# Performance work log

Hardware: AMD Instinct MI355X
Metric: run time of the kernel (lower is better)

The kernel has to match this reference:

```python
import jax, jax.numpy as jnp
import numpy as np

B, S, E, H = 8, 1024, 1024, 16
D = E // H  # head_dim = 64
NEG_INF = jnp.finfo(jnp.float32).min


def setup_inputs() -> dict:
    key = jax.random.key(0)
    ks = jax.random.split(key, 14)
    w = 0.02  # init scale for projection weights
    inp = {
        "query": jax.random.normal(ks[0], (B, S, E), jnp.float32),
        "key": jax.random.normal(ks[1], (B, S, E), jnp.float32),
        "value": jax.random.normal(ks[2], (B, S, E), jnp.float32),
        "attn_bias": jax.random.normal(ks[3], (B, H, S, S), jnp.float32),
        "key_padding_mask": jax.random.randint(ks[4], (B, S), 0, 2).astype(bool),
        "attn_mask": jnp.zeros((S, S), jnp.float32),
        "need_weights": 0,
        "before_softmax": 0,
        "need_head_weights": 0,
        "Wq": jax.random.normal(ks[5], (E, E), jnp.float32) * w,
        "bq": jnp.zeros((E,), jnp.float32),
        "Wk": jax.random.normal(ks[6], (E, E), jnp.float32) * w,
        "bk": jnp.zeros((E,), jnp.float32),
        "Wv": jax.random.normal(ks[7], (E, E), jnp.float32) * w,
        "bv": jnp.zeros((E,), jnp.float32),
        "Wo": jax.random.normal(ks[8], (E, E), jnp.float32) * w,
        "bo": jnp.zeros((E,), jnp.float32),
    }
    return inp


def reference(query, key, value, attn_bias, key_padding_mask, attn_mask,
              need_weights, before_softmax, need_head_weights,
              Wq, bq, Wk, bk, Wv, bv, Wo, bo):
    # self_attention=True: torch code projects q, k, v ALL from `query`.
    scaling = D ** -0.5
    q = (query @ Wq.T + bq) * scaling          # [B,S,E]
    k = query @ Wk.T + bk
    v = query @ Wv.T + bv
    q = q.reshape(B, S, H, D)
    k = k.reshape(B, S, H, D)
    v = v.reshape(B, S, H, D)
    # scores: QK^T + bias + mask, materialized [B,H,S,S] like the torch bmm
    scores = jnp.einsum('bqhd,bkhd->bhqk', q, k)
    scores = scores + attn_bias
    scores = scores + attn_mask[None, None]    # attn_mask broadcast over B,H
    scores = jnp.where(key_padding_mask[:, None, None, :], NEG_INF, scores)
    probs = jax.nn.softmax(scores, axis=-1)    # dropout p=0.0 -> identity
    attn = jnp.einsum('bhqk,bkhd->bqhd', probs, v).reshape(B, S, E)
    out = attn @ Wo.T + bo                     # [B,S,E]
    # need_weights=False path: torch returns (attn, None); return attn only.
    return out
```

## Files before the change

kernel.cpp:

```cpp
#include <hip/hip_runtime.h>

#define B_ 8
#define S_ 1024
#define E_ 1024
#define H_ 16
#define D_ 64

typedef __attribute__((ext_vector_type(8))) short bf16x8;
typedef __attribute__((ext_vector_type(4))) float floatx4;

__device__ __forceinline__ floatx4 mfma16x16x32(bf16x8 a, bf16x8 b, floatx4 c) {
  return __builtin_amdgcn_mfma_f32_16x16x32_bf16(a, b, c, 0, 0, 0);
}

__device__ __forceinline__ unsigned short f2bf(float x) {
  unsigned int u = __builtin_bit_cast(unsigned int, x);
  u += 0x7FFFu + ((u >> 16) & 1u);
  return (unsigned short)(u >> 16);
}

__device__ __forceinline__ void async16(const unsigned short* g, unsigned short* l) {
  __builtin_amdgcn_global_load_lds(
      (const __attribute__((address_space(1))) void*)g,
      (__attribute__((address_space(3))) void*)l, 16, 0, 0);
}

__global__ void mask_prep(const unsigned int* __restrict__ mraw, float* __restrict__ maskadd) {
  __shared__ int flagF, flagB;
  const int tid = threadIdx.x;
  if (tid == 0) { flagF = 0; flagB = 0; }
  __syncthreads();
  int lf = 0, lb = 0;
  for (int i = tid; i < 2048; i += 256) {
    unsigned int v = mraw[i];
    if (v == 0x3F800000u) lf = 1;
    else if (v > 1u) lb = 1;
  }
  if (lf) atomicOr(&flagF, 1);
  if (lb) atomicOr(&flagB, 1);
  __syncthreads();
  const unsigned char* mb = (const unsigned char*)mraw;
  const float* mf = (const float*)mraw;
  const int* mi = (const int*)mraw;
  const int fF = flagF, fB = flagB;
  for (int i = tid; i < B_ * S_; i += 256) {
    int pad;
    if (fF)      pad = (mf[i] != 0.0f);
    else if (fB) pad = (mb[i] != 0);
    else         pad = (mi[i] != 0);
    maskadd[i] = pad ? -3.4028234663852886e38f : 0.0f;
  }
}

__global__ __launch_bounds__(256) void convert_prep(
    const float* __restrict__ q, const float* __restrict__ wq, const float* __restrict__ wk,
    const float* __restrict__ wv, const float* __restrict__ wo,
    unsigned short* __restrict__ xb, unsigned short* __restrict__ wqb,
    unsigned short* __restrict__ wkb, unsigned short* __restrict__ wvb,
    unsigned short* __restrict__ wob)
{
  size_t idx = (size_t)blockIdx.x * 256 + threadIdx.x;
  const float* src; unsigned short* dst; size_t off;
  if (idx < 2097152)      { src = q;  dst = xb;  off = idx; }
  else if (idx < 2359296) { src = wq; dst = wqb; off = idx - 2097152; }
  else if (idx < 2621440) { src = wk; dst = wkb; off = idx - 2359296; }
  else if (idx < 2883584) { src = wv; dst = wvb; off = idx - 2621440; }
  else                    { src = wo; dst = wob; off = idx - 2883584; }
  float4 v = *(const float4*)(src + off * 4);
  ushort4 u; u.x = f2bf(v.x); u.y = f2bf(v.y); u.z = f2bf(v.z); u.w = f2bf(v.w);
  *(ushort4*)(dst + off * 4) = u;
}

__device__ __forceinline__ void gemm_core(
    const unsigned short* __restrict__ A, const unsigned short* __restrict__ Bm,
    int m0, int n0, unsigned short* As, unsigned short* Bs, floatx4 (&acc)[4][4])
{
  const int tid = threadIdx.x;
  const int wave = tid >> 6, lane = tid & 63;
  const int quad = lane >> 4, l16 = lane & 15;
  const int mb = (wave >> 1) * 64, nb = (wave & 1) * 64;
  const int ldrow = lane >> 3;
  const int gchunk = (lane & 7) ^ ldrow;

  for (int ks = 0; ks < 16; ++ks) {
    const int k0 = ks * 64;
    __syncthreads();
    for (int is = 0; is < 4; ++is) {
      int issue = wave * 4 + is;
      async16(A + (size_t)(m0 + issue * 8 + ldrow) * 1024 + k0 + gchunk * 8, &As[issue * 512]);
      async16(Bm + (size_t)(n0 + issue * 8 + ldrow) * 1024 + k0 + gchunk * 8, &Bs[issue * 512]);
    }
    __syncthreads();
    for (int kk = 0; kk < 2; ++kk) {
      const int pc = ((quad + 4 * kk) ^ (l16 & 7)) * 8;
      bf16x8 af[4], bfm[4];
      for (int i = 0; i < 4; ++i)
        af[i] = *(const bf16x8*)(&As[(mb + 16 * i + l16) * 64 + pc]);
      for (int j = 0; j < 4; ++j)
        bfm[j] = *(const bf16x8*)(&Bs[(nb + 16 * j + l16) * 64 + pc]);
      for (int i = 0; i < 4; ++i)
        for (int j = 0; j < 4; ++j)
          acc[i][j] = mfma16x16x32(af[i], bfm[j], acc[i][j]);
    }
  }
}

__global__ __launch_bounds__(256) void gemm_qkv(
    const unsigned short* __restrict__ Xbf,
    const unsigned short* __restrict__ Wqb, const unsigned short* __restrict__ Wkb,
    const unsigned short* __restrict__ Wvb,
    const float* __restrict__ bq, const float* __restrict__ bk, const float* __restrict__ bv,
    unsigned short* __restrict__ qo, unsigned short* __restrict__ ko, unsigned short* __restrict__ vo)
{
  const int n0 = blockIdx.x * 128;
  const int m0 = blockIdx.y * 128;
  const int which = n0 >> 10;
  const int nn0 = n0 & 1023;
  const unsigned short* W = (which == 0) ? Wqb : (which == 1) ? Wkb : Wvb;
  const float* bias = (which == 0) ? bq : (which == 1) ? bk : bv;

  __shared__ unsigned short As[128 * 64];
  __shared__ unsigned short Bs[128 * 64];

  const int lane = threadIdx.x & 63, wave = threadIdx.x >> 6;
  const int quad = lane >> 4, l16 = lane & 15;
  const int mb = (wave >> 1) * 64, nb = (wave & 1) * 64;

  floatx4 z = {0.f, 0.f, 0.f, 0.f};
  floatx4 acc[4][4];
  for (int i = 0; i < 4; ++i) for (int j = 0; j < 4; ++j) acc[i][j] = z;

  gemm_core(Xbf, W, m0, nn0, As, Bs, acc);

  float bv4[4];
  for (int j = 0; j < 4; ++j) bv4[j] = bias[nn0 + nb + 16 * j + l16];

  for (int i = 0; i < 4; ++i) {
    for (int r = 0; r < 4; ++r) {
      int m = m0 + mb + 16 * i + quad * 4 + r;
      int bb = m >> 10, s = m & 1023;
      for (int j = 0; j < 4; ++j) {
        int nn = nn0 + nb + 16 * j + l16;
        int hh = nn >> 6, d = nn & 63;
        float val = acc[i][j][r] + bv4[j];
        if (which == 0) {
          val *= 0.125f;
          qo[((size_t)(bb * 16 + hh) * 1024 + s) * 64 + d] = f2bf(val);
        } else if (which == 1) {
          ko[((size_t)(bb * 16 + hh) * 1024 + s) * 64 + d] = f2bf(val);
        } else {
          vo[((size_t)(bb * 16 + hh) * 64 + d) * 1024 + s] = f2bf(val);
        }
      }
    }
  }
}

__global__ __launch_bounds__(256) void gemm_out(
    const unsigned short* __restrict__ Abf, const unsigned short* __restrict__ Wob,
    const float* __restrict__ bo, float* __restrict__ out)
{
  const int n0 = blockIdx.x * 128;
  const int m0 = blockIdx.y * 128;
  __shared__ unsigned short As[128 * 64];
  __shared__ unsigned short Bs[128 * 64];

  const int lane = threadIdx.x & 63, wave = threadIdx.x >> 6;
  const int quad = lane >> 4, l16 = lane & 15;
  const int mb = (wave >> 1) * 64, nb = (wave & 1) * 64;

  floatx4 z = {0.f, 0.f, 0.f, 0.f};
  floatx4 acc[4][4];
  for (int i = 0; i < 4; ++i) for (int j = 0; j < 4; ++j) acc[i][j] = z;

  gemm_core(Abf, Wob, m0, n0, As, Bs, acc);

  for (int i = 0; i < 4; ++i) {
    for (int r = 0; r < 4; ++r) {
      int m = m0 + mb + 16 * i + quad * 4 + r;
      for (int j = 0; j < 4; ++j) {
        int n = n0 + nb + 16 * j + l16;
        out[(size_t)m * 1024 + n] = acc[i][j][r] + bo[n];
      }
    }
  }
}

__global__ __launch_bounds__(256) void attn_fwd(
    const unsigned short* __restrict__ qw, const unsigned short* __restrict__ kw,
    const unsigned short* __restrict__ vw, const float* __restrict__ bias,
    const float* __restrict__ amask, const float* __restrict__ maskadd,
    unsigned short* __restrict__ attnw)
{
  const int tid = threadIdx.x;
  const int wave = tid >> 6, lane = tid & 63;
  const int quad = lane >> 4, l16 = lane & 15;
  const int qt = blockIdx.x, bh = blockIdx.y;
  const int b = bh >> 4, h = bh & 15;
  const int qbase = qt * 64 + wave * 16;

  const unsigned short* qh = qw + (size_t)bh * (S_ * D_);
  const unsigned short* kh = kw + (size_t)bh * (S_ * D_);
  const unsigned short* vh = vw + (size_t)bh * (S_ * D_);
  const float* biasb = bias + (size_t)bh * ((size_t)S_ * S_) + (size_t)(qt * 64) * S_;
  const float* amrow = amask + (size_t)(qt * 64) * S_;
  const float* madd  = maskadd + b * S_;

  __shared__ float sc[64 * 68];
  __shared__ unsigned short Vt[64 * 64];
  __shared__ unsigned short P_lds[4 * 16 * 72];
  unsigned short* Pw = &P_lds[wave * (16 * 72)];

  const int srow = tid >> 4;
  const int skc  = tid & 15;
  const int vrow = tid >> 3;
  const int vchk = tid & 7;

  bf16x8 aQ0 = *(const bf16x8*)(qh + (size_t)(qbase + l16) * 64 + quad * 8);
  bf16x8 aQ1 = *(const bf16x8*)(qh + (size_t)(qbase + l16) * 64 + 32 + quad * 8);

  float4 pb[4], pa[4], pm;
  bf16x8 pv[2];
  auto load_tile = [&](int key0) {
    pm = *(const float4*)(madd + key0 + skc * 4);
    for (int r4 = 0; r4 < 4; ++r4) {
      pb[r4] = *(const float4*)(biasb + (size_t)(srow + 16 * r4) * S_ + key0 + skc * 4);
      pa[r4] = *(const float4*)(amrow + (size_t)(srow + 16 * r4) * S_ + key0 + skc * 4);
    }
    for (int i2 = 0; i2 < 2; ++i2) {
      int d = vrow + 32 * i2;
      int gc = vchk ^ (d & 7);
      pv[i2] = *(const bf16x8*)(vh + (size_t)d * 1024 + key0 + gc * 8);
    }
  };
  load_tile(0);

  floatx4 zz = {0.f, 0.f, 0.f, 0.f};
  floatx4 oacc[4] = {zz, zz, zz, zz};
  float m_run[4], l_run[4];
  for (int r = 0; r < 4; ++r) { m_run[r] = -__builtin_inff(); l_run[r] = 0.f; }

  for (int kt = 0; kt < 16; ++kt) {
    const int key0 = kt * 64;
    __syncthreads();
    for (int r4 = 0; r4 < 4; ++r4) {
      float4 s;
      s.x = pb[r4].x + pa[r4].x + pm.x;
      s.y = pb[r4].y + pa[r4].y + pm.y;
      s.z = pb[r4].z + pa[r4].z + pm.z;
      s.w = pb[r4].w + pa[r4].w + pm.w;
      *(float4*)(&sc[(srow + 16 * r4) * 68 + skc * 4]) = s;
    }
    for (int i2 = 0; i2 < 2; ++i2)
      *(bf16x8*)(&Vt[(vrow + 32 * i2) * 64 + vchk * 8]) = pv[i2];

    bf16x8 bK0[4], bK1[4];
    for (int t = 0; t < 4; ++t) {
      const unsigned short* kr = kh + (size_t)(key0 + 16 * t + l16) * 64;
      bK0[t] = *(const bf16x8*)(kr + quad * 8);
      bK1[t] = *(const bf16x8*)(kr + 32 + quad * 8);
    }
    if (kt < 15) load_tile(key0 + 64);
    __syncthreads();

    floatx4 sfr[4];
    for (int t = 0; t < 4; ++t) {
      floatx4 c;
      for (int r = 0; r < 4; ++r)
        c[r] = sc[(wave * 16 + quad * 4 + r) * 68 + 16 * t + l16];
      c = mfma16x16x32(aQ0, bK0[t], c);
      c = mfma16x16x32(aQ1, bK1[t], c);
      sfr[t] = c;
    }
    for (int r = 0; r < 4; ++r) {
      float rm = fmaxf(fmaxf(sfr[0][r], sfr[1][r]), fmaxf(sfr[2][r], sfr[3][r]));
      rm = fmaxf(rm, __shfl_xor(rm, 1));
      rm = fmaxf(rm, __shfl_xor(rm, 2));
      rm = fmaxf(rm, __shfl_xor(rm, 4));
      rm = fmaxf(rm, __shfl_xor(rm, 8));
      float mnew = fmaxf(m_run[r], rm);
      float alpha = __expf(m_run[r] - mnew);
      float psum = 0.f;
      for (int t = 0; t < 4; ++t) {
        float p = __expf(sfr[t][r] - mnew);
        psum += p;
        Pw[(quad * 4 + r) * 72 + 16 * t + l16] = f2bf(p);
      }
      psum += __shfl_xor(psum, 1);
      psum += __shfl_xor(psum, 2);
      psum += __shfl_xor(psum, 4);
      psum += __shfl_xor(psum, 8);
      l_run[r] = l_run[r] * alpha + psum;
      m_run[r] = mnew;
      oacc[0][r] *= alpha; oacc[1][r] *= alpha; oacc[2][r] *= alpha; oacc[3][r] *= alpha;
    }
    for (int kc = 0; kc < 2; ++kc) {
      bf16x8 aP = *(const bf16x8*)(Pw + l16 * 72 + kc * 32 + quad * 8);
      const int pc = ((kc * 4 + quad) ^ (l16 & 7)) * 8;
      for (int t = 0; t < 4; ++t) {
        bf16x8 bV = *(const bf16x8*)(&Vt[(16 * t + l16) * 64 + pc]);
        oacc[t] = mfma16x16x32(aP, bV, oacc[t]);
      }
    }
  }

  for (int r = 0; r < 4; ++r) {
    int row = qbase + quad * 4 + r;
    float inv = 1.0f / l_run[r];
    unsigned short* orow = attnw + (size_t)(b * S_ + row) * E_ + h * 64;
    for (int t = 0; t < 4; ++t)
      orow[16 * t + l16] = f2bf(oacc[t][r] * inv);
  }
}

extern "C" void kernel_launch(void* const* d_in, const int* in_sizes, int n_in,
                              void* d_out, int out_size, void* d_ws, size_t ws_size,
                              hipStream_t stream) {
  const float* query      = (const float*)d_in[0];
  const float* attn_bias  = (const float*)d_in[3];
  const unsigned int* kpm = (const unsigned int*)d_in[4];
  const float* amask      = (const float*)d_in[5];
  const float* Wq = (const float*)d_in[9];
  const float* bq = (const float*)d_in[10];
  const float* Wk = (const float*)d_in[11];
  const float* bk = (const float*)d_in[12];
  const float* Wv = (const float*)d_in[13];
  const float* bv = (const float*)d_in[14];
  const float* Wo = (const float*)d_in[15];
  const float* bo = (const float*)d_in[16];

  char* ws = (char*)d_ws;
  const size_t MB16 = 16777216;
  unsigned short* qw    = (unsigned short*)(ws);
  unsigned short* kw    = (unsigned short*)(ws + MB16);
  unsigned short* vw    = (unsigned short*)(ws + 2 * MB16);
  unsigned short* xbf   = (unsigned short*)(ws + 3 * MB16);
  unsigned short* attnw = (unsigned short*)(ws + 3 * MB16);
  unsigned short* wqb   = (unsigned short*)(ws + 4 * MB16);
  unsigned short* wkb   = (unsigned short*)(ws + 4 * MB16 + 2097152);
  unsigned short* wvb   = (unsigned short*)(ws + 4 * MB16 + 2 * 2097152);
  unsigned short* wob   = (unsigned short*)(ws + 4 * MB16 + 3 * 2097152);
  float* maskadd        = (float*)(ws + 4 * MB16 + 4 * 2097152);

  mask_prep<<<1, 256, 0, stream>>>(kpm, maskadd);
  convert_prep<<<12288, 256, 0, stream>>>(query, Wq, Wk, Wv, Wo, xbf, wqb, wkb, wvb, wob);
  gemm_qkv<<<dim3(24, 64), 256, 0, stream>>>(xbf, wqb, wkb, wvb, bq, bk, bv, qw, kw, vw);
  attn_fwd<<<dim3(16, 128), 256, 0, stream>>>(qw, kw, vw, attn_bias, amask, maskadd, attnw);
  gemm_out<<<dim3(8, 64), 256, 0, stream>>>(attnw, wob, bo, (float*)d_out);
}
```

Before: 977.2 us.

## Stage QKV epilogue through LDS, swizzle block order, load bias directly into MFMA layout

The QKV GEMM epilogue now stages the bf16 tile in shared memory (transposed for V) and writes 16-byte vector stores to global, replacing scattered 2-byte stores. All three kernels remap block indices with a swizzle so that neighbouring workgroups are spread across tiles, aimed at L2/XCD locality. The attention kernel drops the LDS score staging buffer and loads bias, mask and padding values straight into registers in the MFMA accumulator layout, double-buffered across key tiles. This costs more registers, and the direct loads are narrower scalar loads than the earlier float4 loads.

```diff
diff --git a/kernel.cpp b/kernel.cpp
--- a/kernel.cpp
+++ b/kernel.cpp
@@ -112,17 +112,22 @@
     const float* __restrict__ bq, const float* __restrict__ bk, const float* __restrict__ bv,
     unsigned short* __restrict__ qo, unsigned short* __restrict__ ko, unsigned short* __restrict__ vo)
 {
-  const int n0 = blockIdx.x * 128;
-  const int m0 = blockIdx.y * 128;
+  const int tid = threadIdx.x;
+  const int flat = blockIdx.y * 24 + blockIdx.x;
+  const int swz = (flat & 7) * 192 + (flat >> 3);
+  const int bx = swz % 24, by = swz / 24;
+  const int n0 = bx * 128;
+  const int m0 = by * 128;
   const int which = n0 >> 10;
   const int nn0 = n0 & 1023;
   const unsigned short* W = (which == 0) ? Wqb : (which == 1) ? Wkb : Wvb;
   const float* bias = (which == 0) ? bq : (which == 1) ? bk : bv;
 
-  __shared__ unsigned short As[128 * 64];
-  __shared__ unsigned short Bs[128 * 64];
-
-  const int lane = threadIdx.x & 63, wave = threadIdx.x >> 6;
+  __shared__ unsigned short smem[128 * 136];
+  unsigned short* As = smem;
+  unsigned short* Bs = smem + 8192;
+
+  const int lane = tid & 63, wave = tid >> 6;
   const int quad = lane >> 4, l16 = lane & 15;
   const int mb = (wave >> 1) * 64, nb = (wave & 1) * 64;
 
@@ -135,24 +140,50 @@
   float bv4[4];
   for (int j = 0; j < 4; ++j) bv4[j] = bias[nn0 + nb + 16 * j + l16];
 
-  for (int i = 0; i < 4; ++i) {
-    for (int r = 0; r < 4; ++r) {
-      int m = m0 + mb + 16 * i + quad * 4 + r;
-      int bb = m >> 10, s = m & 1023;
-      for (int j = 0; j < 4; ++j) {
-        int nn = nn0 + nb + 16 * j + l16;
-        int hh = nn >> 6, d = nn & 63;
-        float val = acc[i][j][r] + bv4[j];
-        if (which == 0) {
-          val *= 0.125f;
-          qo[((size_t)(bb * 16 + hh) * 1024 + s) * 64 + d] = f2bf(val);
-        } else if (which == 1) {
-          ko[((size_t)(bb * 16 + hh) * 1024 + s) * 64 + d] = f2bf(val);
-        } else {
-          vo[((size_t)(bb * 16 + hh) * 64 + d) * 1024 + s] = f2bf(val);
-        }
-      }
-    }
+  __syncthreads();
+
+  const float scale = (which == 0) ? 0.125f : 1.0f;
+  if (which < 2) {
+    #pragma unroll
+    for (int i = 0; i < 4; ++i)
+      #pragma unroll
+      for (int r = 0; r < 4; ++r) {
+        const int mr = mb + 16 * i + quad * 4 + r;
+        #pragma unroll
+        for (int j = 0; j < 4; ++j)
+          smem[mr * 136 + nb + 16 * j + l16] = f2bf((acc[i][j][r] + bv4[j]) * scale);
+      }
+  } else {
+    #pragma unroll
+    for (int i = 0; i < 4; ++i)
+      #pragma unroll
+      for (int r = 0; r < 4; ++r) {
+        const int mr = mb + 16 * i + quad * 4 + r;
+        #pragma unroll
+        for (int j = 0; j < 4; ++j)
+          smem[(nb + 16 * j + l16) * 136 + mr] = f2bf(acc[i][j][r] + bv4[j]);
+      }
+  }
+  __syncthreads();
+
+  const int row = tid >> 1, half = tid & 1;
+  if (which < 2) {
+    const int m = m0 + row, bb = m >> 10, s = m & 1023;
+    const int hh = (nn0 >> 6) + half;
+    unsigned short* dst = ((which == 0) ? qo : ko) +
+        ((size_t)(bb * 16 + hh) * 1024 + s) * 64;
+    #pragma unroll
+    for (int c = 0; c < 8; ++c)
+      *(bf16x8*)(dst + c * 8) = *(const bf16x8*)(&smem[row * 136 + half * 64 + c * 8]);
+  } else {
+    const int nglob = nn0 + row;
+    const int hh = nglob >> 6, d = nglob & 63;
+    const int bb = m0 >> 10;
+    unsigned short* dst = vo + ((size_t)(bb * 16 + hh) * 64 + d) * 1024 +
+        (m0 & 1023) + half * 64;
+    #pragma unroll
+    for (int c = 0; c < 8; ++c)
+      *(bf16x8*)(dst + c * 8) = *(const bf16x8*)(&smem[row * 136 + half * 64 + c * 8]);
   }
 }
 
@@ -160,8 +191,10 @@
     const unsigned short* __restrict__ Abf, const unsigned short* __restrict__ Wob,
     const float* __restrict__ bo, float* __restrict__ out)
 {
-  const int n0 = blockIdx.x * 128;
-  const int m0 = blockIdx.y * 128;
+  const int flat = blockIdx.y * 8 + blockIdx.x;
+  const int swz = (flat & 7) * 64 + (flat >> 3);
+  const int n0 = (swz & 7) * 128;
+  const int m0 = (swz >> 3) * 128;
   __shared__ unsigned short As[128 * 64];
   __shared__ unsigned short Bs[128 * 64];
 
@@ -195,45 +228,53 @@
   const int tid = threadIdx.x;
   const int wave = tid >> 6, lane = tid & 63;
   const int quad = lane >> 4, l16 = lane & 15;
-  const int qt = blockIdx.x, bh = blockIdx.y;
+  const int flat = blockIdx.y * 16 + blockIdx.x;
+  const int swz = (flat & 7) * 256 + (flat >> 3);
+  const int qt = swz & 15, bh = swz >> 4;
   const int b = bh >> 4, h = bh & 15;
   const int qbase = qt * 64 + wave * 16;
 
   const unsigned short* qh = qw + (size_t)bh * (S_ * D_);
   const unsigned short* kh = kw + (size_t)bh * (S_ * D_);
   const unsigned short* vh = vw + (size_t)bh * (S_ * D_);
-  const float* biasb = bias + (size_t)bh * ((size_t)S_ * S_) + (size_t)(qt * 64) * S_;
-  const float* amrow = amask + (size_t)(qt * 64) * S_;
+  const float* biasb = bias + (size_t)bh * ((size_t)S_ * S_) +
+                       (size_t)(qt * 64 + wave * 16 + quad * 4) * S_;
+  const float* amrow = amask + (size_t)(qt * 64 + wave * 16 + quad * 4) * S_;
   const float* madd  = maskadd + b * S_;
 
-  __shared__ float sc[64 * 68];
   __shared__ unsigned short Vt[64 * 64];
   __shared__ unsigned short P_lds[4 * 16 * 72];
   unsigned short* Pw = &P_lds[wave * (16 * 72)];
 
-  const int srow = tid >> 4;
-  const int skc  = tid & 15;
   const int vrow = tid >> 3;
   const int vchk = tid & 7;
 
   bf16x8 aQ0 = *(const bf16x8*)(qh + (size_t)(qbase + l16) * 64 + quad * 8);
   bf16x8 aQ1 = *(const bf16x8*)(qh + (size_t)(qbase + l16) * 64 + 32 + quad * 8);
 
-  float4 pb[4], pa[4], pm;
   bf16x8 pv[2];
-  auto load_tile = [&](int key0) {
-    pm = *(const float4*)(madd + key0 + skc * 4);
-    for (int r4 = 0; r4 < 4; ++r4) {
-      pb[r4] = *(const float4*)(biasb + (size_t)(srow + 16 * r4) * S_ + key0 + skc * 4);
-      pa[r4] = *(const float4*)(amrow + (size_t)(srow + 16 * r4) * S_ + key0 + skc * 4);
-    }
+  float cc[4][4], nc[4][4];
+
+  auto load_v = [&](int key0) {
+    #pragma unroll
     for (int i2 = 0; i2 < 2; ++i2) {
       int d = vrow + 32 * i2;
       int gc = vchk ^ (d & 7);
       pv[i2] = *(const bf16x8*)(vh + (size_t)d * 1024 + key0 + gc * 8);
     }
   };
-  load_tile(0);
+  auto load_cinit = [&](int key0, float (&dst)[4][4]) {
+    #pragma unroll
+    for (int t = 0; t < 4; ++t) {
+      const int col = key0 + 16 * t + l16;
+      const float mv = madd[col];
+      #pragma unroll
+      for (int r = 0; r < 4; ++r)
+        dst[t][r] = biasb[(size_t)r * S_ + col] + amrow[(size_t)r * S_ + col] + mv;
+    }
+  };
+  load_v(0);
+  load_cinit(0, cc);
 
   floatx4 zz = {0.f, 0.f, 0.f, 0.f};
   floatx4 oacc[4] = {zz, zz, zz, zz};
@@ -243,35 +284,31 @@
   for (int kt = 0; kt < 16; ++kt) {
     const int key0 = kt * 64;
     __syncthreads();
-    for (int r4 = 0; r4 < 4; ++r4) {
-      float4 s;
-      s.x = pb[r4].x + pa[r4].x + pm.x;
-      s.y = pb[r4].y + pa[r4].y + pm.y;
-      s.z = pb[r4].z + pa[r4].z + pm.z;
-      s.w = pb[r4].w + pa[r4].w + pm.w;
-      *(float4*)(&sc[(srow + 16 * r4) * 68 + skc * 4]) = s;
-    }
+    #pragma unroll
     for (int i2 = 0; i2 < 2; ++i2)
       *(bf16x8*)(&Vt[(vrow + 32 * i2) * 64 + vchk * 8]) = pv[i2];
 
     bf16x8 bK0[4], bK1[4];
+    #pragma unroll
     for (int t = 0; t < 4; ++t) {
       const unsigned short* kr = kh + (size_t)(key0 + 16 * t + l16) * 64;
       bK0[t] = *(const bf16x8*)(kr + quad * 8);
       bK1[t] = *(const bf16x8*)(kr + 32 + quad * 8);
     }
-    if (kt < 15) load_tile(key0 + 64);
+    if (kt < 15) { load_v(key0 + 64); load_cinit(key0 + 64, nc); }
     __syncthreads();
 
     floatx4 sfr[4];
+    #pragma unroll
     for (int t = 0; t < 4; ++t) {
       floatx4 c;
-      for (int r = 0; r < 4; ++r)
-        c[r] = sc[(wave * 16 + quad * 4 + r) * 68 + 16 * t + l16];
+      #pragma unroll
+      for (int r = 0; r < 4; ++r) c[r] = cc[t][r];
       c = mfma16x16x32(aQ0, bK0[t], c);
       c = mfma16x16x32(aQ1, bK1[t], c);
       sfr[t] = c;
     }
+    #pragma unroll
     for (int r = 0; r < 4; ++r) {
       float rm = fmaxf(fmaxf(sfr[0][r], sfr[1][r]), fmaxf(sfr[2][r], sfr[3][r]));
       rm = fmaxf(rm, __shfl_xor(rm, 1));
@@ -281,6 +318,7 @@
       float mnew = fmaxf(m_run[r], rm);
       float alpha = __expf(m_run[r] - mnew);
       float psum = 0.f;
+      #pragma unroll
       for (int t = 0; t < 4; ++t) {
         float p = __expf(sfr[t][r] - mnew);
         psum += p;
@@ -294,13 +332,21 @@
       m_run[r] = mnew;
       oacc[0][r] *= alpha; oacc[1][r] *= alpha; oacc[2][r] *= alpha; oacc[3][r] *= alpha;
     }
+    #pragma unroll
     for (int kc = 0; kc < 2; ++kc) {
       bf16x8 aP = *(const bf16x8*)(Pw + l16 * 72 + kc * 32 + quad * 8);
       const int pc = ((kc * 4 + quad) ^ (l16 & 7)) * 8;
+      #pragma unroll
       for (int t = 0; t < 4; ++t) {
         bf16x8 bV = *(const bf16x8*)(&Vt[(16 * t + l16) * 64 + pc]);
         oacc[t] = mfma16x16x32(aP, bV, oacc[t]);
       }
+    }
+    if (kt < 15) {
+      #pragma unroll
+      for (int t = 0; t < 4; ++t)
+        #pragma unroll
+        for (int r = 0; r < 4; ++r) cc[t][r] = nc[t][r];
     }
   }
 
```

Measured after the change: 984.8 us. Within noise of the previous version (+0.8%).
